# Optimization experiments

Measured on AMD Instinct MI355X. Metric: run time of the kernel, lower is better.

Reference implementation:

```python
import jax, jax.numpy as jnp
import numpy as np

B, T, F, U, L = 64, 512, 256, 1024, 3
LN_EPS = 1e-12  # tf.contrib.layers.layer_norm default


def setup_inputs() -> dict:
    key = jax.random.key(0)
    ks = jax.random.split(key, 8)

    def w(k, shape):
        return jax.random.normal(k, shape, jnp.float32) / np.float32(np.sqrt(shape[0]))

    return {
        "input": jax.random.normal(ks[0], (B, T, F), jnp.float32),
        "conditioned_lst": jax.random.randint(ks[1], (T,), 0, 2).astype(bool),
        # LSTM layer 0: input = feature F, layers 1..2: input = U
        "W0": w(ks[2], (F + U, 4 * U)), "b0": jnp.zeros((4 * U,), jnp.float32),
        "W1": w(ks[3], (2 * U, 4 * U)), "b1": jnp.zeros((4 * U,), jnp.float32),
        "W2": w(ks[4], (2 * U, 4 * U)), "b2": jnp.zeros((4 * U,), jnp.float32),
        # output dense projection back to feature dim
        "Wd": w(ks[5], (U, F)), "bd": jnp.zeros((F,), jnp.float32),
        # layer norm params
        "gamma": jnp.ones((F,), jnp.float32), "beta": jnp.zeros((F,), jnp.float32),
    }


def _lstm_cell(x, h, c, W, b):
    # BasicLSTMCell: gates in (i, j, f, o) order, forget_bias = 1.0
    z = jnp.dot(jnp.concatenate([x, h], axis=-1), W) + b
    i, j, f, o = jnp.split(z, 4, axis=-1)
    c_new = c * jax.nn.sigmoid(f + 1.0) + jax.nn.sigmoid(i) * jnp.tanh(j)
    h_new = jax.nn.sigmoid(o) * jnp.tanh(c_new)
    return h_new, c_new


def reference(input, conditioned_lst, W0, b0, W1, b1, W2, b2, Wd, bd, gamma, beta):
    Ws, bs = [W0, W1, W2], [b0, b1, b2]
    xs = (jnp.arange(T), jnp.swapaxes(input, 0, 1), conditioned_lst)  # time-major
    carry0 = (jnp.zeros((L, B, U), input.dtype),  # h per layer
              jnp.zeros((L, B, U), input.dtype),  # c per layer
              jnp.zeros((B, F), input.dtype))     # previous emit

    def step(carry, xt):
        hs, cs, prev_emit = carry
        t, x_t, cond_t = xt
        # auto-conditioning: teacher-force on conditioned steps (and step 0)
        x = jnp.where(jnp.logical_or(t == 0, cond_t), x_t, prev_emit)
        new_h, new_c = [], []
        for l in range(L):
            h, c = _lstm_cell(x, hs[l], cs[l], Ws[l], bs[l])
            new_h.append(h)
            new_c.append(c)
            x = h
        y = jnp.dot(x, Wd) + bd  # dense projection [B, F]
        mu = jnp.mean(y, axis=-1, keepdims=True)
        var = jnp.mean(jnp.square(y - mu), axis=-1, keepdims=True)
        y = (y - mu) * jax.lax.rsqrt(var + LN_EPS) * gamma + beta
        emit = jax.nn.relu(y)
        return (jnp.stack(new_h), jnp.stack(new_c), emit), emit

    _, outs = jax.lax.scan(step, carry0, xs)  # [T, B, F]
    return jnp.swapaxes(outs, 0, 1)  # [B, T, F]
```

## Files before the change

### kernel.cpp

```cpp
#include <hip/hip_runtime.h>
#include <math.h>

#define B 64
#define T 512
#define F 256
#define U 1024
#define NBLK 256
#define NTH 512
#define WPAD 68

typedef unsigned short ushort_t;
typedef __attribute__((ext_vector_type(8))) _Float16 f16x8_t;
typedef __attribute__((ext_vector_type(4))) float f32x4_t;

static const size_t OFF_STATS= 0;
static const size_t OFF_COND = 4096;
static const size_t OFF_BAR  = 6144;
static const size_t OFF_H2B  = 7424;
static const size_t OFF_HS   = 269568;
static const size_t OFF_YB   = 1056000;
static const size_t OFF_PW0  = 1088768;
static const size_t OFF_PW1  = 11574528;
static const size_t OFF_PW2  = 28351744;
static const size_t ZERO_BYTES = OFF_PW0;

__device__ __forceinline__ float sigm(float x) {
    return 1.0f / (1.0f + __expf(-x));
}

__device__ __forceinline__ ushort_t f2h(float x) {
    _Float16 h = (_Float16)x;
    union { _Float16 h; ushort_t u; } v; v.h = h;
    return v.u;
}
__device__ __forceinline__ float h2f(ushort_t u) {
    union { ushort_t u; _Float16 h; } v; v.u = u;
    return (float)v.h;
}

__device__ __forceinline__ void store_uc_u16(ushort_t* p, ushort_t v) {
    asm volatile("global_store_short %0, %1, off sc0 sc1"
                 :: "v"(p), "v"((unsigned)v) : "memory");
}
__device__ __forceinline__ void store_uc_f32(float* p, float v) {
    asm volatile("global_store_dword %0, %1, off sc0 sc1"
                 :: "v"(p), "v"(v) : "memory");
}
__device__ __forceinline__ void store_uc_b64(void* p, unsigned long long v) {
    asm volatile("global_store_dwordx2 %0, %1, off sc0 sc1"
                 :: "v"(p), "v"(v) : "memory");
}
__device__ __forceinline__ void drain_vmem() {
    asm volatile("s_waitcnt vmcnt(0)" ::: "memory");
}

__device__ __forceinline__ void phase_sync(int* bar, int epoch, int g) {
    drain_vmem();
    __syncthreads();
    if (threadIdx.x == 0) {
        const int sub = g & 7;
        const int prev = __hip_atomic_fetch_add(bar + sub * 16, 1,
                                                __ATOMIC_RELAXED, __HIP_MEMORY_SCOPE_AGENT);
        if (prev == epoch * 32 - 1) {
            const int pm = __hip_atomic_fetch_add(bar + 128, 1,
                                                  __ATOMIC_RELAXED, __HIP_MEMORY_SCOPE_AGENT);
            if (pm == epoch * 8 - 1) {
                #pragma unroll
                for (int i = 0; i < 8; ++i)
                    __hip_atomic_store(bar + 144 + i * 16, epoch, __ATOMIC_RELAXED,
                                       __HIP_MEMORY_SCOPE_AGENT);
            }
        }
        int* myrelay = bar + 144 + sub * 16;
        int spins = 0;
        while (__hip_atomic_load(myrelay, __ATOMIC_RELAXED,
                                 __HIP_MEMORY_SCOPE_AGENT) < epoch) {
            __builtin_amdgcn_s_sleep(1);
            if ((++spins & 255) == 0)
                (void)__hip_atomic_load(myrelay, __ATOMIC_ACQUIRE,
                                        __HIP_MEMORY_SCOPE_AGENT);
        }
    }
    __syncthreads();
}

__global__ void prep_kernel(const unsigned char* __restrict__ condraw,
                            unsigned char* __restrict__ wsb) {
    __shared__ int s_not_int32;
    const int tid = threadIdx.x;
    if (tid == 0) s_not_int32 = 0;
    __syncthreads();
    if (tid < 512 && (tid & 3) != 0) {
        if (condraw[tid] != 0) s_not_int32 = 1;
    }
    __syncthreads();
    const int is32 = (s_not_int32 == 0);
    int* condw = (int*)(wsb + OFF_COND);
    if (tid < 512) {
        int cv = is32 ? ((const int*)condraw)[tid] : (int)condraw[tid];
        condw[tid] = (cv != 0) ? 1 : 0;
    }
}

__global__ void repack_kernel(const float* __restrict__ W0,
                              const float* __restrict__ W1,
                              const float* __restrict__ W2,
                              unsigned char* __restrict__ wsb) {
    ushort_t* P0 = (ushort_t*)(wsb + OFF_PW0);
    ushort_t* P1 = (ushort_t*)(wsb + OFF_PW1);
    ushort_t* P2 = (ushort_t*)(wsb + OFF_PW2);
    const size_t stride = (size_t)gridDim.x * blockDim.x;
    const size_t tid = (size_t)blockIdx.x * blockDim.x + threadIdx.x;
    const size_t N0 = (size_t)256 * 40 * 512;
    const size_t N12 = (size_t)256 * 64 * 512;
    for (size_t i = tid; i < N0; i += stride) {
        const int g = (int)(i / 20480);
        const int r = (int)(i % 20480);
        const int kt = r >> 9, s = r & 511, L = s >> 3, j = s & 7;
        const int k = kt * 32 + ((L >> 4) << 3) + j;
        const int n = L & 15;
        const int col = ((n >> 2) << 10) + (g << 2) + (n & 3);
        P0[i] = f2h(W0[(size_t)k * 4096 + col]);
    }
    for (size_t i = tid; i < N12; i += stride) {
        const int g = (int)(i / 32768);
        const int r = (int)(i % 32768);
        const int kt = r >> 9, s = r & 511, L = s >> 3, j = s & 7;
        const int k = kt * 32 + ((L >> 4) << 3) + j;
        const int n = L & 15;
        const int col = ((n >> 2) << 10) + (g << 2) + (n & 3);
        const size_t src = (size_t)k * 4096 + col;
        P1[i] = f2h(W1[src]);
        P2[i] = f2h(W2[src]);
    }
}

__global__ void __launch_bounds__(NTH, 2)
lstm_persistent(const float* __restrict__ input,
                const float* __restrict__ b0, const float* __restrict__ b1,
                const float* __restrict__ b2,
                const float* __restrict__ Wd, const float* __restrict__ bd,
                const float* __restrict__ gamma, const float* __restrict__ beta,
                float* __restrict__ out, unsigned char* __restrict__ wsb) {
    const int g = blockIdx.x;
    const int tid = threadIdx.x;
    const int lane = tid & 63;
    const int wv = __builtin_amdgcn_readfirstlane(tid >> 6);
    const int ln15 = lane & 15;
    const int quad = lane >> 4;

    float* h2b = (float*)(wsb + OFF_H2B);
    float* stats = (float*)(wsb + OFF_STATS);
    int* bar = (int*)(wsb + OFF_BAR);
    ushort_t* hs = (ushort_t*)(wsb + OFF_HS);
    ushort_t* yb = (ushort_t*)(wsb + OFF_YB);
    const size_t HSZ = (size_t)256 * 64 * 4;

    __shared__ f16x8_t lds_pw0[40 * 64];
    __shared__ f32x4_t lds_wd4[1024];
    __shared__ float zbuf[128 * WPAD];
    __shared__ float zbuf2[128];
    __shared__ int lds_cond[512];

    const int u0 = g << 2;
    const int f0 = g << 2;
    const int k0 = (wv << 5) + (quad << 3);
    const int fb0 = k0 >> 2;

    f16x8_t Bw1[8], Bw2[8];
    {
        const ushort_t* p1 = (const ushort_t*)(wsb + OFF_PW1) +
                             (size_t)g * 64 * 512 + (size_t)lane * 8;
        const ushort_t* p2 = (const ushort_t*)(wsb + OFF_PW2) +
                             (size_t)g * 64 * 512 + (size_t)lane * 8;
        #pragma unroll
        for (int i = 0; i < 4; ++i) {
            Bw1[i]     = *(const f16x8_t*)(p1 + (size_t)((wv << 2) + i) * 512);
            Bw1[4 + i] = *(const f16x8_t*)(p1 + (size_t)(32 + (wv << 2) + i) * 512);
            Bw2[i]     = *(const f16x8_t*)(p2 + (size_t)((wv << 2) + i) * 512);
            Bw2[4 + i] = *(const f16x8_t*)(p2 + (size_t)(32 + (wv << 2) + i) * 512);
        }
    }
    {
        const f16x8_t* src = (const f16x8_t*)((const ushort_t*)(wsb + OFF_PW0) +
                                              (size_t)g * 40 * 512);
        for (int i = tid; i < 40 * 64; i += NTH) lds_pw0[i] = src[i];
    }
    if (g < 64) {
        for (int k = tid; k < 1024; k += NTH)
            lds_wd4[k] = *(const f32x4_t*)(Wd + (size_t)k * F + f0);
    }
    for (int i = tid; i < 512; i += NTH) lds_cond[i] = ((const int*)(wsb + OFF_COND))[i];

    const int eb = tid >> 2;
    const int eu = tid & 3;

    float bias0[4], bias1[4], bias2[4];
    if (tid < 256) {
        #pragma unroll
        for (int q = 0; q < 4; ++q) {
            bias0[q] = b0[(q << 10) + u0 + eu];
            bias1[q] = b1[(q << 10) + u0 + eu];
            bias2[q] = b2[(q << 10) + u0 + eu];
        }
    }
    float gmv[8], btv[8];
    {
        const float4 g0 = *(const float4*)(gamma + k0);
        const float4 g1 = *(const float4*)(gamma + k0 + 4);
        const float4 t0 = *(const float4*)(beta + k0);
        const float4 t1 = *(const float4*)(beta + k0 + 4);
        gmv[0]=g0.x; gmv[1]=g0.y; gmv[2]=g0.z; gmv[3]=g0.w;
        gmv[4]=g1.x; gmv[5]=g1.y; gmv[6]=g1.z; gmv[7]=g1.w;
        btv[0]=t0.x; btv[1]=t0.y; btv[2]=t0.z; btv[3]=t0.w;
        btv[4]=t1.x; btv[5]=t1.y; btv[6]=t1.z; btv[7]=t1.w;
    }
    float4 gm4 = {0,0,0,0}, bt4 = {0,0,0,0}, bd4 = {0,0,0,0};
    if (g < 64 && wv == 1) {
        gm4 = *(const float4*)(gamma + f0);
        bt4 = *(const float4*)(beta + f0);
    }
    if (g < 64 && wv == 0) {
        bd4 = *(const float4*)(bd + f0);
    }
    __syncthreads();

    float creg0 = 0.f, creg1 = 0.f, creg2 = 0.f;

    f32x4_t acc0[4], acc1[4], acc2[4];
    #pragma unroll
    for (int mt = 0; mt < 4; ++mt) {
        acc0[mt] = (f32x4_t){0.f, 0.f, 0.f, 0.f};
        acc1[mt] = (f32x4_t){0.f, 0.f, 0.f, 0.f};
        acc2[mt] = (f32x4_t){0.f, 0.f, 0.f, 0.f};
    }

    auto ld_frag = [&](const char* p) -> f16x8_t {
        union { unsigned long long q[2]; f16x8_t v; } u;
        u.q[0] = *(const unsigned long long*)(p);
        u.q[1] = *(const unsigned long long*)(p + 512);
        return u.v;
    };

    auto mm4 = [&](f32x4_t (&acc)[4], const ushort_t* base,
                   const f16x8_t (&Bw)[8], const int boff) {
        f16x8_t Ab[4][4];
        const char* bb = (const char*)base + (size_t)ln15 * 8 +
                         (size_t)(quad << 1) * 512;
        #pragma unroll
        for (int c = 0; c < 4; ++c) {
            const char* pc = bb + (size_t)((wv << 2) + c) * 4096;
            #pragma unroll
            for (int mt = 0; mt < 4; ++mt)
                Ab[c][mt] = ld_frag(pc + mt * 128);
        }
        #pragma unroll
        for (int c = 0; c < 4; ++c) {
            #pragma unroll
            for (int mt = 0; mt < 4; ++mt)
                acc[mt] = __builtin_amdgcn_mfma_f32_16x16x32_f16(
                    Ab[c][mt], Bw[boff + c], acc[mt], 0, 0, 0);
        }
    };

    auto mm_h0 = [&](f32x4_t (&acc)[4], const ushort_t* base) {
        f16x8_t Ab[4][4];
        const char* bb = (const char*)base + (size_t)ln15 * 8 +
                         (size_t)(quad << 1) * 512;
        #pragma unroll
        for (int c = 0; c < 4; ++c) {
            const char* pc = bb + (size_t)((wv << 2) + c) * 4096;
            #pragma unroll
            for (int mt = 0; mt < 4; ++mt)
                Ab[c][mt] = ld_frag(pc + mt * 128);
        }
        #pragma unroll
        for (int c = 0; c < 4; ++c) {
            const f16x8_t Bb = lds_pw0[(8 + (wv << 2) + c) * 64 + lane];
            #pragma unroll
            for (int mt = 0; mt < 4; ++mt)
                acc[mt] = __builtin_amdgcn_mfma_f32_16x16x32_f16(
                    Ab[c][mt], Bb, acc[mt], 0, 0, 0);
        }
    };

    auto epilogue = [&](f32x4_t (&acc)[4], const float (&bi)[4], float& cr,
                        ushort_t* hdst, float* h2dst) {
        __syncthreads();
        {
            float* zrow = zbuf + (size_t)(wv * 16 + ln15) * WPAD;
            #pragma unroll
            for (int mt = 0; mt < 4; ++mt)
                *(f32x4_t*)(zrow + mt * 16 + (quad << 2)) = acc[mt];
            #pragma unroll
            for (int mt = 0; mt < 4; ++mt) acc[mt] = (f32x4_t){0.f, 0.f, 0.f, 0.f};
        }
        __syncthreads();
        if (tid < 256) {
            float z[4];
            #pragma unroll
            for (int q = 0; q < 4; ++q) {
                float s = bi[q];
                #pragma unroll
                for (int w = 0; w < 8; ++w)
                    s += zbuf[(size_t)(w * 16 + q * 4 + eu) * WPAD + eb];
                z[q] = s;
            }
            const float ig = sigm(z[0]);
            const float gg = tanhf(z[1]);
            const float fg = sigm(z[2] + 1.0f);
            const float og = sigm(z[3]);
            const float cn = cr * fg + ig * gg;
            const float hn = og * tanhf(cn);
            cr = cn;
            store_uc_u16(hdst + (size_t)g * 256 + tid, f2h(hn));
            if (h2dst) store_uc_f32(h2dst + (size_t)g * 256 + tid, hn);
        }
    };

    int epoch = 0;
    for (int t = 0; t < T; ++t) {
        const int p = t & 1;
        const int pn = p ^ 1;
        ushort_t* hs0n = hs + (size_t)(pn * 3 + 0) * HSZ;
        ushort_t* hs1n = hs + (size_t)(pn * 3 + 1) * HSZ;
        ushort_t* hs2n = hs + (size_t)(pn * 3 + 2) * HSZ;

        __builtin_amdgcn_fence(__ATOMIC_ACQUIRE, "agent");

        if (g < 64) {
            mm4(acc1, hs + (size_t)(p * 3 + 1) * HSZ, Bw1, 4);
            mm4(acc2, hs + (size_t)(p * 3 + 2) * HSZ, Bw2, 4);
        }
        if (tid < 64) {
            const float2 sv = *(const float2*)(stats + (size_t)pn * (64 * 8) + tid * 8);
            const float mu = sv.x * (1.0f / F);
            const float var = sv.y * (1.0f / F) - mu * mu;
            zbuf2[tid * 2] = mu;
            zbuf2[tid * 2 + 1] = rsqrtf(var + 1e-12f);
        }
        __syncthreads();
        if (g < 64 && wv == 1 && t > 0) {
            union { unsigned long long q; ushort_t s[4]; } yq;
            yq.q = *(const unsigned long long*)(yb + ((size_t)g * 64 + lane) * 4);
            const float mu = zbuf2[lane * 2], rs = zbuf2[lane * 2 + 1];
            float4 o;
            o.x = fmaxf((h2f(yq.s[0]) - mu) * rs * gm4.x + bt4.x, 0.0f);
            o.y = fmaxf((h2f(yq.s[1]) - mu) * rs * gm4.y + bt4.y, 0.0f);
            o.z = fmaxf((h2f(yq.s[2]) - mu) * rs * gm4.z + bt4.z, 0.0f);
            o.w = fmaxf((h2f(yq.s[3]) - mu) * rs * gm4.w + bt4.w, 0.0f);
            *(float4*)(out + (size_t)lane * (T * F) + (size_t)(t - 1) * F + f0) = o;
        }
        {
            const int condt = (t == 0) || (lds_cond[t] != 0);
            f16x8_t Ax[4];
            #pragma unroll
            for (int mt = 0; mt < 4; ++mt) {
                const int b = ln15 + (mt << 4);
                union { ushort_t s[8]; f16x8_t v; } ux;
                if (condt) {
                    const float* ip = input + (size_t)b * (T * F) + (size_t)t * F + k0;
                    const float4 a0 = *(const float4*)(ip);
                    const float4 a1 = *(const float4*)(ip + 4);
                    ux.s[0] = f2h(a0.x); ux.s[1] = f2h(a0.y);
                    ux.s[2] = f2h(a0.z); ux.s[3] = f2h(a0.w);
                    ux.s[4] = f2h(a1.x); ux.s[5] = f2h(a1.y);
                    ux.s[6] = f2h(a1.z); ux.s[7] = f2h(a1.w);
                } else {
                    union { unsigned long long q; ushort_t s[4]; } y0, y1;
                    y0.q = *(const unsigned long long*)(yb + ((size_t)fb0 * 64 + b) * 4);
                    y1.q = *(const unsigned long long*)(yb + ((size_t)(fb0 + 1) * 64 + b) * 4);
                    const float mu = zbuf2[b * 2], rs = zbuf2[b * 2 + 1];
                    #pragma unroll
                    for (int j = 0; j < 4; ++j) {
                        ux.s[j] = f2h(fmaxf((h2f(y0.s[j]) - mu) * rs * gmv[j] + btv[j], 0.0f));
                        ux.s[4 + j] = f2h(fmaxf((h2f(y1.s[j]) - mu) * rs * gmv[4 + j] + btv[4 + j], 0.0f));
                    }
                }
                Ax[mt] = ux.v;
            }
            const f16x8_t Bb = lds_pw0[wv * 64 + lane];
            #pragma unroll
            for (int mt = 0; mt < 4; ++mt)
                acc0[mt] = __builtin_amdgcn_mfma_f32_16x16x32_f16(
                    Ax[mt], Bb, acc0[mt], 0, 0, 0);
        }
        epilogue(acc0, bias0, creg0, hs0n, nullptr);
        phase_sync(bar, ++epoch, g);

        mm4(acc1, hs0n, Bw1, 0);
        if (g < 64) mm_h0(acc0, hs0n);
        epilogue(acc1, bias1, creg1, hs1n, nullptr);
        phase_sync(bar, ++epoch, g);

        mm4(acc2, hs1n, Bw2, 0);
        epilogue(acc2, bias2, creg2, hs2n, h2b);
        phase_sync(bar, ++epoch, g);

        if (g < 64) {
            float accd[4] = {0.f, 0.f, 0.f, 0.f};
            #pragma unroll
            for (int half = 0; half < 2; ++half) {
                f32x4_t hv[16];
                const f32x4_t* hb4 = (const f32x4_t*)h2b +
                    (size_t)(wv * 32 + half * 16) * 64 + lane;
                #pragma unroll
                for (int i = 0; i < 16; ++i)
                    hv[i] = hb4[(size_t)i * 64];
                #pragma unroll
                for (int i = 0; i < 16; ++i) {
                    const int k = (wv << 7) + (half << 6) + (i << 2);
                    #pragma unroll
                    for (int j = 0; j < 4; ++j) {
                        const f32x4_t w4 = lds_wd4[k + j];
                        accd[0] = fmaf(w4[0], hv[i][j], accd[0]);
                        accd[1] = fmaf(w4[1], hv[i][j], accd[1]);
                        accd[2] = fmaf(w4[2], hv[i][j], accd[2]);
                        accd[3] = fmaf(w4[3], hv[i][j], accd[3]);
                    }
                }
            }
            __syncthreads();
            #pragma unroll
            for (int jj = 0; jj < 4; ++jj)
                zbuf[(size_t)(wv * 16 + jj) * WPAD + lane] = accd[jj];
            __syncthreads();
            if (wv == 0) {
                float yv[4];
                float s = 0.f, ss = 0.f;
                #pragma unroll
                for (int jj = 0; jj < 4; ++jj) {
                    float y = 0.f;
                    #pragma unroll
                    for (int w = 0; w < 8; ++w)
                        y += zbuf[(size_t)(w * 16 + jj) * WPAD + lane];
                    y += (jj == 0) ? bd4.x : (jj == 1) ? bd4.y : (jj == 2) ? bd4.z : bd4.w;
                    yv[jj] = y;
                    s += y;
                    ss += y * y;
                }
                unsigned long long pk =
                    (unsigned long long)f2h(yv[0]) |
                    ((unsigned long long)f2h(yv[1]) << 16) |
                    ((unsigned long long)f2h(yv[2]) << 32) |
                    ((unsigned long long)f2h(yv[3]) << 48);
                store_uc_b64(yb + ((size_t)g * 64 + lane) * 4, pk);
                float* st = stats + (size_t)p * (64 * 8);
                atomicAdd(&st[(size_t)lane * 8], s);
                atomicAdd(&st[(size_t)lane * 8 + 1], ss);
            }
        } else if (g == 64 && wv == 0) {
            float* st2 = stats + (size_t)pn * (64 * 8);
            store_uc_b64(&st2[(size_t)lane * 8], 0ULL);
        }

        if (g >= 64 && t + 1 < T) {
            mm_h0(acc0, hs0n);
            mm4(acc1, hs1n, Bw1, 4);
            mm4(acc2, hs2n, Bw2, 4);
        }
        phase_sync(bar, ++epoch, g);
    }

    if (g < 64) {
        __builtin_amdgcn_fence(__ATOMIC_ACQUIRE, "agent");
        if (tid < 64) {
            const float2 sv = *(const float2*)(stats + (size_t)((T - 1) & 1) * (64 * 8) + tid * 8);
            const float mu = sv.x * (1.0f / F);
            const float var = sv.y * (1.0f / F) - mu * mu;
            zbuf2[tid * 2] = mu;
            zbuf2[tid * 2 + 1] = rsqrtf(var + 1e-12f);
        }
        __syncthreads();
        if (wv == 1) {
            union { unsigned long long q; ushort_t s[4]; } yq;
            yq.q = *(const unsigned long long*)(yb + ((size_t)g * 64 + lane) * 4);
            const float mu = zbuf2[lane * 2], rs = zbuf2[lane * 2 + 1];
            float4 o;
            o.x = fmaxf((h2f(yq.s[0]) - mu) * rs * gm4.x + bt4.x, 0.0f);
            o.y = fmaxf((h2f(yq.s[1]) - mu) * rs * gm4.y + bt4.y, 0.0f);
            o.z = fmaxf((h2f(yq.s[2]) - mu) * rs * gm4.z + bt4.z, 0.0f);
            o.w = fmaxf((h2f(yq.s[3]) - mu) * rs * gm4.w + bt4.w, 0.0f);
            *(float4*)(out + (size_t)lane * (T * F) + (size_t)(T - 1) * F + f0) = o;
        }
    }
}

extern "C" void kernel_launch(void* const* d_in, const int* in_sizes, int n_in,
                              void* d_out, int out_size, void* d_ws, size_t ws_size,
                              hipStream_t stream) {
    const float* input = (const float*)d_in[0];
    const unsigned char* condraw = (const unsigned char*)d_in[1];
    const float* W0 = (const float*)d_in[2];
    const float* b0 = (const float*)d_in[3];
    const float* W1 = (const float*)d_in[4];
    const float* b1 = (const float*)d_in[5];
    const float* W2 = (const float*)d_in[6];
    const float* b2 = (const float*)d_in[7];
    const float* Wd = (const float*)d_in[8];
    const float* bd = (const float*)d_in[9];
    const float* gamma = (const float*)d_in[10];
    const float* beta = (const float*)d_in[11];
    float* out = (float*)d_out;
    unsigned char* wsb = (unsigned char*)d_ws;

    hipMemsetAsync(d_ws, 0, ZERO_BYTES, stream);
    prep_kernel<<<1, 512, 0, stream>>>(condraw, wsb);
    repack_kernel<<<2048, 256, 0, stream>>>(W0, W1, W2, wsb);
    lstm_persistent<<<NBLK, NTH, 0, stream>>>(input, b0, b1, b2, Wd, bd,
                                              gamma, beta, out, wsb);
}
```

Before: 25.59 ms.

## Fuse recurrent-h matmuls into input-h passes and vectorize h stores

The recurrent contributions for layers 0 and 1 at the next step are now computed in the same pass that loads the fresh hidden-state fragments (dual MFMA loops sharing A fragments), instead of in separate passes at the end of the step. The epilogue stages h through LDS so one wave emits packed 64-bit f16 stores and 128-bit f32 stores instead of per-thread scalar uncached stores. Input and emit loads are hoisted ahead of the layer-2 recurrent matmul to overlap their latency. This shortens the work on the critical path between barriers but adds an extra __syncthreads in each epilogue and more live registers.

```diff
diff --git a/kernel.cpp b/kernel.cpp
--- a/kernel.cpp
+++ b/kernel.cpp
@@ -38,16 +38,12 @@
     return (float)v.h;
 }
 
-__device__ __forceinline__ void store_uc_u16(ushort_t* p, ushort_t v) {
-    asm volatile("global_store_short %0, %1, off sc0 sc1"
-                 :: "v"(p), "v"((unsigned)v) : "memory");
-}
-__device__ __forceinline__ void store_uc_f32(float* p, float v) {
-    asm volatile("global_store_dword %0, %1, off sc0 sc1"
-                 :: "v"(p), "v"(v) : "memory");
-}
 __device__ __forceinline__ void store_uc_b64(void* p, unsigned long long v) {
     asm volatile("global_store_dwordx2 %0, %1, off sc0 sc1"
+                 :: "v"(p), "v"(v) : "memory");
+}
+__device__ __forceinline__ void store_uc_b128(void* p, f32x4_t v) {
+    asm volatile("global_store_dwordx4 %0, %1, off sc0 sc1"
                  :: "v"(p), "v"(v) : "memory");
 }
 __device__ __forceinline__ void drain_vmem() {
@@ -160,6 +156,7 @@
     __shared__ f32x4_t lds_wd4[1024];
     __shared__ float zbuf[128 * WPAD];
     __shared__ float zbuf2[128];
+    __shared__ float hbuf[64 * 5];
     __shared__ int lds_cond[512];
 
     const int u0 = g << 2;
@@ -192,16 +189,16 @@
     }
     for (int i = tid; i < 512; i += NTH) lds_cond[i] = ((const int*)(wsb + OFF_COND))[i];
 
-    const int eb = tid >> 2;
-    const int eu = tid & 3;
+    const int ebo = tid & 63;
+    const int euo = (tid >> 6) & 3;
 
     float bias0[4], bias1[4], bias2[4];
     if (tid < 256) {
         #pragma unroll
         for (int q = 0; q < 4; ++q) {
-            bias0[q] = b0[(q << 10) + u0 + eu];
-            bias1[q] = b1[(q << 10) + u0 + eu];
-            bias2[q] = b2[(q << 10) + u0 + eu];
+            bias0[q] = b0[(q << 10) + u0 + euo];
+            bias1[q] = b1[(q << 10) + u0 + euo];
+            bias2[q] = b2[(q << 10) + u0 + euo];
         }
     }
     float gmv[8], btv[8];
@@ -263,7 +260,9 @@
         }
     };
 
-    auto mm_h0 = [&](f32x4_t (&acc)[4], const ushort_t* base) {
+    auto mm4_dual_reg = [&](f32x4_t (&accX)[4], const f16x8_t (&BwX)[8],
+                            f32x4_t (&accH)[4], const f16x8_t (&BwH)[8],
+                            const ushort_t* base) {
         f16x8_t Ab[4][4];
         const char* bb = (const char*)base + (size_t)ln15 * 8 +
                          (size_t)(quad << 1) * 512;
@@ -276,11 +275,39 @@
         }
         #pragma unroll
         for (int c = 0; c < 4; ++c) {
-            const f16x8_t Bb = lds_pw0[(8 + (wv << 2) + c) * 64 + lane];
-            #pragma unroll
-            for (int mt = 0; mt < 4; ++mt)
-                acc[mt] = __builtin_amdgcn_mfma_f32_16x16x32_f16(
-                    Ab[c][mt], Bb, acc[mt], 0, 0, 0);
+            #pragma unroll
+            for (int mt = 0; mt < 4; ++mt)
+                accX[mt] = __builtin_amdgcn_mfma_f32_16x16x32_f16(
+                    Ab[c][mt], BwX[c], accX[mt], 0, 0, 0);
+            #pragma unroll
+            for (int mt = 0; mt < 4; ++mt)
+                accH[mt] = __builtin_amdgcn_mfma_f32_16x16x32_f16(
+                    Ab[c][mt], BwH[4 + c], accH[mt], 0, 0, 0);
+        }
+    };
+    auto mm4_dual_lds0 = [&](f32x4_t (&accX)[4], const f16x8_t (&BwX)[8],
+                             f32x4_t (&accH)[4], const ushort_t* base) {
+        f16x8_t Ab[4][4];
+        const char* bb = (const char*)base + (size_t)ln15 * 8 +
+                         (size_t)(quad << 1) * 512;
+        #pragma unroll
+        for (int c = 0; c < 4; ++c) {
+            const char* pc = bb + (size_t)((wv << 2) + c) * 4096;
+            #pragma unroll
+            for (int mt = 0; mt < 4; ++mt)
+                Ab[c][mt] = ld_frag(pc + mt * 128);
+        }
+        #pragma unroll
+        for (int c = 0; c < 4; ++c) {
+            const f16x8_t Bh = lds_pw0[(8 + (wv << 2) + c) * 64 + lane];
+            #pragma unroll
+            for (int mt = 0; mt < 4; ++mt)
+                accX[mt] = __builtin_amdgcn_mfma_f32_16x16x32_f16(
+                    Ab[c][mt], BwX[c], accX[mt], 0, 0, 0);
+            #pragma unroll
+            for (int mt = 0; mt < 4; ++mt)
+                accH[mt] = __builtin_amdgcn_mfma_f32_16x16x32_f16(
+                    Ab[c][mt], Bh, accH[mt], 0, 0, 0);
         }
     };
 
@@ -303,7 +330,7 @@
                 float s = bi[q];
                 #pragma unroll
                 for (int w = 0; w < 8; ++w)
-                    s += zbuf[(size_t)(w * 16 + q * 4 + eu) * WPAD + eb];
+                    s += zbuf[(size_t)(w * 16 + q * 4 + euo) * WPAD + ebo];
                 z[q] = s;
             }
             const float ig = sigm(z[0]);
@@ -313,8 +340,27 @@
             const float cn = cr * fg + ig * gg;
             const float hn = og * tanhf(cn);
             cr = cn;
-            store_uc_u16(hdst + (size_t)g * 256 + tid, f2h(hn));
-            if (h2dst) store_uc_f32(h2dst + (size_t)g * 256 + tid, hn);
+            hbuf[ebo * 5 + euo] = hn;
+        }
+        __syncthreads();
+        if (wv == 0) {
+            const float h0v = hbuf[lane * 5 + 0];
+            const float h1v = hbuf[lane * 5 + 1];
+            const float h2v = hbuf[lane * 5 + 2];
+            const float h3v = hbuf[lane * 5 + 3];
+            unsigned long long pk =
+                (unsigned long long)f2h(h0v) |
+                ((unsigned long long)f2h(h1v) << 16) |
+                ((unsigned long long)f2h(h2v) << 32) |
+                ((unsigned long long)f2h(h3v) << 48);
+            store_uc_b64(hdst + (size_t)g * 256 + lane * 4, pk);
+        } else if (wv == 1 && h2dst) {
+            f32x4_t v;
+            v[0] = hbuf[lane * 5 + 0];
+            v[1] = hbuf[lane * 5 + 1];
+            v[2] = hbuf[lane * 5 + 2];
+            v[3] = hbuf[lane * 5 + 3];
+            store_uc_b128(h2dst + (size_t)g * 256 + lane * 4, v);
         }
     };
 
@@ -328,21 +374,49 @@
 
         __builtin_amdgcn_fence(__ATOMIC_ACQUIRE, "agent");
 
-        if (g < 64) {
-            mm4(acc1, hs + (size_t)(p * 3 + 1) * HSZ, Bw1, 4);
+        const int condt = (t == 0) || (lds_cond[t] != 0);
+        unsigned long long xr0[4], xr1[4];
+        if (condt) {
+            #pragma unroll
+            for (int mt = 0; mt < 4; ++mt) {
+                const int b = ln15 + (mt << 4);
+                const float* ip = input + (size_t)b * (T * F) + (size_t)t * F + k0;
+                const float4 a0 = *(const float4*)(ip);
+                const float4 a1 = *(const float4*)(ip + 4);
+                xr0[mt] = (unsigned long long)f2h(a0.x) |
+                          ((unsigned long long)f2h(a0.y) << 16) |
+                          ((unsigned long long)f2h(a0.z) << 32) |
+                          ((unsigned long long)f2h(a0.w) << 48);
+                xr1[mt] = (unsigned long long)f2h(a1.x) |
+                          ((unsigned long long)f2h(a1.y) << 16) |
+                          ((unsigned long long)f2h(a1.z) << 32) |
+                          ((unsigned long long)f2h(a1.w) << 48);
+            }
+        } else {
+            #pragma unroll
+            for (int mt = 0; mt < 4; ++mt) {
+                const int b = ln15 + (mt << 4);
+                xr0[mt] = *(const unsigned long long*)(yb + ((size_t)fb0 * 64 + b) * 4);
+                xr1[mt] = *(const unsigned long long*)(yb + ((size_t)(fb0 + 1) * 64 + b) * 4);
+            }
+        }
+        unsigned long long yqe = 0;
+        if (g < 64 && wv == 1 && t > 0)
+            yqe = *(const unsigned long long*)(yb + ((size_t)g * 64 + lane) * 4);
+        float2 svst = {0.f, 0.f};
+        if (tid < 64)
+            svst = *(const float2*)(stats + (size_t)pn * (64 * 8) + tid * 8);
+        if (g < 64)
             mm4(acc2, hs + (size_t)(p * 3 + 2) * HSZ, Bw2, 4);
-        }
         if (tid < 64) {
-            const float2 sv = *(const float2*)(stats + (size_t)pn * (64 * 8) + tid * 8);
-            const float mu = sv.x * (1.0f / F);
-            const float var = sv.y * (1.0f / F) - mu * mu;
+            const float mu = svst.x * (1.0f / F);
+            const float var = svst.y * (1.0f / F) - mu * mu;
             zbuf2[tid * 2] = mu;
             zbuf2[tid * 2 + 1] = rsqrtf(var + 1e-12f);
         }
         __syncthreads();
         if (g < 64 && wv == 1 && t > 0) {
-            union { unsigned long long q; ushort_t s[4]; } yq;
-            yq.q = *(const unsigned long long*)(yb + ((size_t)g * 64 + lane) * 4);
+            union { unsigned long long q; ushort_t s[4]; } yq; yq.q = yqe;
             const float mu = zbuf2[lane * 2], rs = zbuf2[lane * 2 + 1];
             float4 o;
             o.x = fmaxf((h2f(yq.s[0]) - mu) * rs * gm4.x + bt4.x, 0.0f);
@@ -352,24 +426,17 @@
             *(float4*)(out + (size_t)lane * (T * F) + (size_t)(t - 1) * F + f0) = o;
         }
         {
-            const int condt = (t == 0) || (lds_cond[t] != 0);
             f16x8_t Ax[4];
             #pragma unroll
             for (int mt = 0; mt < 4; ++mt) {
-                const int b = ln15 + (mt << 4);
-                union { ushort_t s[8]; f16x8_t v; } ux;
+                union { unsigned long long q[2]; f16x8_t v;
+                        ushort_t s[8]; } ux;
                 if (condt) {
-                    const float* ip = input + (size_t)b * (T * F) + (size_t)t * F + k0;
-                    const float4 a0 = *(const float4*)(ip);
-                    const float4 a1 = *(const float4*)(ip + 4);
-                    ux.s[0] = f2h(a0.x); ux.s[1] = f2h(a0.y);
-                    ux.s[2] = f2h(a0.z); ux.s[3] = f2h(a0.w);
-                    ux.s[4] = f2h(a1.x); ux.s[5] = f2h(a1.y);
-                    ux.s[6] = f2h(a1.z); ux.s[7] = f2h(a1.w);
+                    ux.q[0] = xr0[mt]; ux.q[1] = xr1[mt];
                 } else {
+                    const int b = ln15 + (mt << 4);
                     union { unsigned long long q; ushort_t s[4]; } y0, y1;
-                    y0.q = *(const unsigned long long*)(yb + ((size_t)fb0 * 64 + b) * 4);
-                    y1.q = *(const unsigned long long*)(yb + ((size_t)(fb0 + 1) * 64 + b) * 4);
+                    y0.q = xr0[mt]; y1.q = xr1[mt];
                     const float mu = zbuf2[b * 2], rs = zbuf2[b * 2 + 1];
                     #pragma unroll
                     for (int j = 0; j < 4; ++j) {
@@ -388,12 +455,11 @@
         epilogue(acc0, bias0, creg0, hs0n, nullptr);
         phase_sync(bar, ++epoch, g);
 
-        mm4(acc1, hs0n, Bw1, 0);
-        if (g < 64) mm_h0(acc0, hs0n);
+        mm4_dual_lds0(acc1, Bw1, acc0, hs0n);
         epilogue(acc1, bias1, creg1, hs1n, nullptr);
         phase_sync(bar, ++epoch, g);
 
-        mm4(acc2, hs1n, Bw2, 0);
+        mm4_dual_reg(acc2, Bw2, acc1, Bw1, hs1n);
         epilogue(acc2, bias2, creg2, hs2n, h2b);
         phase_sync(bar, ++epoch, g);
 
@@ -453,12 +519,8 @@
             float* st2 = stats + (size_t)pn * (64 * 8);
             store_uc_b64(&st2[(size_t)lane * 8], 0ULL);
         }
-
-        if (g >= 64 && t + 1 < T) {
-            mm_h0(acc0, hs0n);
-            mm4(acc1, hs1n, Bw1, 4);
+        if (g >= 64 && t + 1 < T)
             mm4(acc2, hs2n, Bw2, 4);
-        }
         phase_sync(bar, ++epoch, g);
     }
 
```

Result: faster. 24.12 ms (-5.7%).
